# Performance work log

Hardware: AMD Instinct MI355X
Metric: run time of the kernel (lower is better)

## Reference

```python
import jax, jax.numpy as jnp
import numpy as np

E = 800_000
N = 50_000
NUM_RADIAL = 6
HIDDEN = 256
OUT_EMB = 192
OUT = 1
NUM_LAYERS = 3


def setup_inputs() -> dict:
    key = jax.random.key(0)
    ks = jax.random.split(key, 10)
    s = lambda fan_in: 1.0 / np.sqrt(fan_in)
    inp = {
        "x": jax.random.normal(ks[0], (E, HIDDEN), dtype=jnp.float32),
        "rbf": jax.random.normal(ks[1], (E, NUM_RADIAL), dtype=jnp.float32),
        "i": jax.random.randint(ks[2], (E,), 0, N, dtype=jnp.int64),
        "num_nodes": N,
        # params
        "W_rbf": jax.random.normal(ks[3], (NUM_RADIAL, HIDDEN), dtype=jnp.float32) * s(NUM_RADIAL),
        "W_up": jax.random.normal(ks[4], (HIDDEN, OUT_EMB), dtype=jnp.float32) * s(HIDDEN),
        "b_up": jnp.zeros((OUT_EMB,), dtype=jnp.float32),
        "W_lins": jax.random.normal(ks[5], (NUM_LAYERS, OUT_EMB, OUT_EMB), dtype=jnp.float32) * s(OUT_EMB),
        "b_lins": jnp.zeros((NUM_LAYERS, OUT_EMB), dtype=jnp.float32),
        "W_out": jax.random.normal(ks[6], (OUT_EMB, OUT), dtype=jnp.float32) * s(OUT_EMB),
    }
    return inp


def reference(x, rbf, i, num_nodes, W_rbf, W_up, b_up, W_lins, b_lins, W_out):
    # edge module: gate edge features by rbf projection
    g = jnp.matmul(rbf, W_rbf)          # [E, H]
    xe = g * x                          # [E, H]
    # scatter-add edges -> nodes
    xn = jax.ops.segment_sum(xe, i, num_segments=num_nodes)  # [N, H]
    # node MLP
    h = jnp.matmul(xn, W_up) + b_up     # [N, OUT_EMB]
    for l in range(W_lins.shape[0]):
        h = jax.nn.silu(jnp.matmul(h, W_lins[l]) + b_lins[l])
    return jnp.matmul(h, W_out)         # [N, OUT]
```

## Files before the change

### kernel.cpp

```cpp
#include <hip/hip_runtime.h>
#include <cmath>

#define HIDDEN 256
#define NUM_RADIAL 6
#define OUT_EMB 192
#define NUM_LAYERS 3
#define TN 32


__global__ __launch_bounds__(256) void hist_kernel(const int* __restrict__ idx,
                                                   int* __restrict__ counts, int E) {
    const int e = blockIdx.x * 256 + threadIdx.x;
    if (e < E) atomicAdd(&counts[idx[e]], 1);
}

__global__ __launch_bounds__(1024) void scan_kernel(const int* __restrict__ counts,
                                                    int* __restrict__ start,
                                                    int* __restrict__ cursor,
                                                    int N, int E) {
    __shared__ int pref[1024];
    const int t = threadIdx.x;
    const int chunk = (N + 1023) >> 10;
    const int lo = min(t * chunk, N), hi = min(lo + chunk, N);
    int s = 0;
    for (int i = lo; i < hi; i++) s += counts[i];
    pref[t] = s;
    __syncthreads();
    if (t == 0) {
        int run = 0;
        for (int i = 0; i < 1024; i++) { const int v = pref[i]; pref[i] = run; run += v; }
    }
    __syncthreads();
    int run = pref[t];
    for (int i = lo; i < hi; i++) {
        start[i] = run; cursor[i] = run; run += counts[i];
    }
    if (t == 0) start[N] = E;
}

__global__ __launch_bounds__(256) void perm_kernel(const int* __restrict__ idx,
                                                   int* __restrict__ cursor,
                                                   int* __restrict__ perm, int E) {
    const int e = blockIdx.x * 256 + threadIdx.x;
    if (e < E) {
        const int pos = atomicAdd(&cursor[idx[e]], 1);
        perm[pos] = e;
    }
}

__global__ __launch_bounds__(256) void gather_kernel(
    const float* __restrict__ x, const float* __restrict__ rbf,
    const int* __restrict__ perm, const int* __restrict__ start,
    const float* __restrict__ W_rbf, float* __restrict__ xn, int N)
{
    const int n = blockIdx.x;
    const int c = threadIdx.x;

    float wr[NUM_RADIAL];
    #pragma unroll
    for (int r = 0; r < NUM_RADIAL; r++) wr[r] = W_rbf[r * HIDDEN + c];

    const int p0 = start[n], p1 = start[n + 1];
    float acc = 0.f;
    for (int p = p0; p < p1; p++) {
        const int e = perm[p];
        float g = 0.f;
        #pragma unroll
        for (int r = 0; r < NUM_RADIAL; r++)
            g += wr[r] * rbf[(size_t)e * NUM_RADIAL + r];
        acc += g * x[(size_t)e * HIDDEN + c];
    }
    xn[(size_t)n * HIDDEN + c] = acc;
}


__global__ __launch_bounds__(192) void node_mlp(
    const float* __restrict__ xn,
    const float* __restrict__ W_up, const float* __restrict__ b_up,
    const float* __restrict__ W_lins, const float* __restrict__ b_lins,
    const float* __restrict__ W_out,
    float* __restrict__ out, int N)
{
    __shared__ float xl[TN * HIDDEN];
    __shared__ float hl[TN * OUT_EMB];
    const int j = threadIdx.x;
    const int nbase = blockIdx.x * TN;

    for (int t = j; t < TN * HIDDEN; t += 192) {
        const int n = t / HIDDEN;
        xl[t] = (nbase + n < N) ? xn[(size_t)(nbase + n) * HIDDEN + (t & (HIDDEN - 1))]
                                : 0.f;
    }
    __syncthreads();

    float acc[TN];

    {
        const float bj = b_up[j];
        #pragma unroll
        for (int n = 0; n < TN; n++) acc[n] = bj;
        for (int c0 = 0; c0 < HIDDEN; c0 += 32) {
            float w[32];
            #pragma unroll
            for (int k = 0; k < 32; k++) w[k] = W_up[(c0 + k) * OUT_EMB + j];
            #pragma unroll
            for (int k = 0; k < 32; k += 4) {
                #pragma unroll
                for (int n = 0; n < TN; n++) {
                    const float4 xv = *(const float4*)&xl[n * HIDDEN + c0 + k];
                    acc[n] += xv.x * w[k] + xv.y * w[k + 1] + xv.z * w[k + 2] + xv.w * w[k + 3];
                }
            }
        }
        __syncthreads();
        #pragma unroll
        for (int n = 0; n < TN; n++) hl[n * OUT_EMB + j] = acc[n];
        __syncthreads();
    }

    for (int l = 0; l < NUM_LAYERS; l++) {
        const float* __restrict__ W = W_lins + (size_t)l * OUT_EMB * OUT_EMB;
        const float bj = b_lins[l * OUT_EMB + j];
        #pragma unroll
        for (int n = 0; n < TN; n++) acc[n] = bj;
        for (int c0 = 0; c0 < OUT_EMB; c0 += 32) {
            float w[32];
            #pragma unroll
            for (int k = 0; k < 32; k++) w[k] = W[(c0 + k) * OUT_EMB + j];
            #pragma unroll
            for (int k = 0; k < 32; k += 4) {
                #pragma unroll
                for (int n = 0; n < TN; n++) {
                    const float4 hv = *(const float4*)&hl[n * OUT_EMB + c0 + k];
                    acc[n] += hv.x * w[k] + hv.y * w[k + 1] + hv.z * w[k + 2] + hv.w * w[k + 3];
                }
            }
        }
        __syncthreads();
        #pragma unroll
        for (int n = 0; n < TN; n++) {
            const float a = acc[n];
            hl[n * OUT_EMB + j] = a / (1.f + __expf(-a));
        }
        __syncthreads();
    }

    if (j < TN && nbase + j < N) {
        float s = 0.f;
        for (int c = 0; c < OUT_EMB; c++) s += hl[j * OUT_EMB + c] * W_out[c];
        out[nbase + j] = s;
    }
}

extern "C" void kernel_launch(void* const* d_in, const int* in_sizes, int n_in,
                              void* d_out, int out_size, void* d_ws, size_t ws_size,
                              hipStream_t stream) {
    const float* x      = (const float*)d_in[0];
    const float* rbf    = (const float*)d_in[1];
    const int*   idx    = (const int*)d_in[2];
    const float* W_rbf  = (const float*)d_in[4];
    const float* W_up   = (const float*)d_in[5];
    const float* b_up   = (const float*)d_in[6];
    const float* W_lins = (const float*)d_in[7];
    const float* b_lins = (const float*)d_in[8];
    const float* W_out  = (const float*)d_in[9];
    float* out = (float*)d_out;

    const int E = in_sizes[2];
    const int N = out_size;

    char* ws = (char*)d_ws;
    float* xn     = (float*)ws;                    ws += (size_t)N * HIDDEN * sizeof(float);
    int*   counts = (int*)ws;                      ws += (size_t)N * sizeof(int);
    int*   start  = (int*)ws;                      ws += (size_t)(N + 1) * sizeof(int);
    int*   cursor = (int*)ws;                      ws += (size_t)N * sizeof(int);
    int*   perm   = (int*)ws;

    hipMemsetAsync(counts, 0, (size_t)N * sizeof(int), stream);
    const int eblocks = (E + 255) / 256;
    hist_kernel<<<eblocks, 256, 0, stream>>>(idx, counts, E);
    scan_kernel<<<1, 1024, 0, stream>>>(counts, start, cursor, N, E);
    perm_kernel<<<eblocks, 256, 0, stream>>>(idx, cursor, perm, E);
    gather_kernel<<<N, 256, 0, stream>>>(x, rbf, perm, start, W_rbf, xn, N);

    node_mlp<<<(N + TN - 1) / TN, 192, 0, stream>>>(xn, W_up, b_up, W_lins, b_lins,
                                                    W_out, out, N);
}
```

Before: 2.155 ms.

## Vectorize gather per wavefront and retile node MLP with register blocking

The gather kernel now assigns one 64-lane wavefront per node, with each lane handling four channels through float4 loads, and processes two edges per iteration to expose more memory parallelism. The node MLP switches to 256 threads, where each thread computes an 8-node by 3-output register tile. The first layer reads xn directly from global memory instead of staging it in shared memory, which cuts the LDS footprint. The final output projection is split across 8 lanes per node and reduced with shuffles, replacing the mostly idle 32-thread serial loop. The trade-off is higher register pressure, and the up-projection now depends on global or cache reads of xn rather than LDS.

```diff
diff --git a/kernel.cpp b/kernel.cpp
--- a/kernel.cpp
+++ b/kernel.cpp
@@ -5,7 +5,10 @@
 #define NUM_RADIAL 6
 #define OUT_EMB 192
 #define NUM_LAYERS 3
-#define TN 32
+
+#define TM 32
+#define NPG 8
+#define JT 3
 
 
 __global__ __launch_bounds__(256) void hist_kernel(const int* __restrict__ idx,
@@ -48,107 +51,178 @@
     }
 }
 
+__device__ __forceinline__ float4 edge_term(const float rv0, const float rv1,
+                                            const float rv2, const float rv3,
+                                            const float rv4, const float rv5,
+                                            const float4* wr, const float4 xv) {
+    float4 g;
+    g.x = rv0*wr[0].x + rv1*wr[1].x + rv2*wr[2].x + rv3*wr[3].x + rv4*wr[4].x + rv5*wr[5].x;
+    g.y = rv0*wr[0].y + rv1*wr[1].y + rv2*wr[2].y + rv3*wr[3].y + rv4*wr[4].y + rv5*wr[5].y;
+    g.z = rv0*wr[0].z + rv1*wr[1].z + rv2*wr[2].z + rv3*wr[3].z + rv4*wr[4].z + rv5*wr[5].z;
+    g.w = rv0*wr[0].w + rv1*wr[1].w + rv2*wr[2].w + rv3*wr[3].w + rv4*wr[4].w + rv5*wr[5].w;
+    return make_float4(g.x*xv.x, g.y*xv.y, g.z*xv.z, g.w*xv.w);
+}
+
 __global__ __launch_bounds__(256) void gather_kernel(
     const float* __restrict__ x, const float* __restrict__ rbf,
     const int* __restrict__ perm, const int* __restrict__ start,
     const float* __restrict__ W_rbf, float* __restrict__ xn, int N)
 {
-    const int n = blockIdx.x;
-    const int c = threadIdx.x;
-
-    float wr[NUM_RADIAL];
+    const int lane = threadIdx.x & 63;
+    const int slot = threadIdx.x >> 6;
+    const int n = blockIdx.x * 4 + slot;
+    if (n >= N) return;
+    const int c0 = lane << 2;
+
+    float4 wr[NUM_RADIAL];
     #pragma unroll
-    for (int r = 0; r < NUM_RADIAL; r++) wr[r] = W_rbf[r * HIDDEN + c];
+    for (int r = 0; r < NUM_RADIAL; r++)
+        wr[r] = *(const float4*)&W_rbf[r * HIDDEN + c0];
 
     const int p0 = start[n], p1 = start[n + 1];
-    float acc = 0.f;
-    for (int p = p0; p < p1; p++) {
-        const int e = perm[p];
-        float g = 0.f;
-        #pragma unroll
-        for (int r = 0; r < NUM_RADIAL; r++)
-            g += wr[r] * rbf[(size_t)e * NUM_RADIAL + r];
-        acc += g * x[(size_t)e * HIDDEN + c];
-    }
-    xn[(size_t)n * HIDDEN + c] = acc;
-}
-
-
-__global__ __launch_bounds__(192) void node_mlp(
+    float4 acc = make_float4(0.f, 0.f, 0.f, 0.f);
+
+    int p = p0;
+    for (; p + 2 <= p1; p += 2) {
+        const int e0 = perm[p];
+        const int e1 = perm[p + 1];
+        const float2* rb0 = (const float2*)(rbf + (size_t)e0 * NUM_RADIAL);
+        const float2* rb1 = (const float2*)(rbf + (size_t)e1 * NUM_RADIAL);
+        const float2 a0 = rb0[0], a1 = rb0[1], a2 = rb0[2];
+        const float2 b0 = rb1[0], b1 = rb1[1], b2 = rb1[2];
+        const float4 xv0 = *(const float4*)&x[(size_t)e0 * HIDDEN + c0];
+        const float4 xv1 = *(const float4*)&x[(size_t)e1 * HIDDEN + c0];
+        const float4 t0 = edge_term(a0.x, a0.y, a1.x, a1.y, a2.x, a2.y, wr, xv0);
+        const float4 t1 = edge_term(b0.x, b0.y, b1.x, b1.y, b2.x, b2.y, wr, xv1);
+        acc.x += t0.x + t1.x; acc.y += t0.y + t1.y;
+        acc.z += t0.z + t1.z; acc.w += t0.w + t1.w;
+    }
+    if (p < p1) {
+        const int e0 = perm[p];
+        const float2* rb0 = (const float2*)(rbf + (size_t)e0 * NUM_RADIAL);
+        const float2 a0 = rb0[0], a1 = rb0[1], a2 = rb0[2];
+        const float4 xv0 = *(const float4*)&x[(size_t)e0 * HIDDEN + c0];
+        const float4 t0 = edge_term(a0.x, a0.y, a1.x, a1.y, a2.x, a2.y, wr, xv0);
+        acc.x += t0.x; acc.y += t0.y; acc.z += t0.z; acc.w += t0.w;
+    }
+    *(float4*)&xn[(size_t)n * HIDDEN + c0] = acc;
+}
+
+
+__global__ __launch_bounds__(256, 4) void node_mlp(
     const float* __restrict__ xn,
     const float* __restrict__ W_up, const float* __restrict__ b_up,
     const float* __restrict__ W_lins, const float* __restrict__ b_lins,
     const float* __restrict__ W_out,
     float* __restrict__ out, int N)
 {
-    __shared__ float xl[TN * HIDDEN];
-    __shared__ float hl[TN * OUT_EMB];
-    const int j = threadIdx.x;
-    const int nbase = blockIdx.x * TN;
-
-    for (int t = j; t < TN * HIDDEN; t += 192) {
-        const int n = t / HIDDEN;
-        xl[t] = (nbase + n < N) ? xn[(size_t)(nbase + n) * HIDDEN + (t & (HIDDEN - 1))]
-                                : 0.f;
-    }
-    __syncthreads();
-
-    float acc[TN];
+    __shared__ float hl[TM * OUT_EMB];
+    const int t = threadIdx.x;
+    const int j = t & 63;
+    const int g = t >> 6;
+    const int nbase = blockIdx.x * TM;
+    const int n0 = g * NPG;
+
+    float acc[NPG][JT];
+
+    const float* xrow[NPG];
+    #pragma unroll
+    for (int n = 0; n < NPG; n++) {
+        int nn = nbase + n0 + n;
+        if (nn > N - 1) nn = N - 1;
+        xrow[n] = xn + (size_t)nn * HIDDEN;
+    }
 
     {
-        const float bj = b_up[j];
-        #pragma unroll
-        for (int n = 0; n < TN; n++) acc[n] = bj;
-        for (int c0 = 0; c0 < HIDDEN; c0 += 32) {
-            float w[32];
-            #pragma unroll
-            for (int k = 0; k < 32; k++) w[k] = W_up[(c0 + k) * OUT_EMB + j];
-            #pragma unroll
-            for (int k = 0; k < 32; k += 4) {
-                #pragma unroll
-                for (int n = 0; n < TN; n++) {
-                    const float4 xv = *(const float4*)&xl[n * HIDDEN + c0 + k];
-                    acc[n] += xv.x * w[k] + xv.y * w[k + 1] + xv.z * w[k + 2] + xv.w * w[k + 3];
+        float bj[JT];
+        #pragma unroll
+        for (int m = 0; m < JT; m++) bj[m] = b_up[j + 64 * m];
+        #pragma unroll
+        for (int n = 0; n < NPG; n++)
+            #pragma unroll
+            for (int m = 0; m < JT; m++) acc[n][m] = bj[m];
+
+        for (int c0 = 0; c0 < HIDDEN; c0 += 8) {
+            float w[8][JT];
+            #pragma unroll
+            for (int k = 0; k < 8; k++)
+                #pragma unroll
+                for (int m = 0; m < JT; m++)
+                    w[k][m] = W_up[(c0 + k) * OUT_EMB + j + 64 * m];
+            #pragma unroll
+            for (int n = 0; n < NPG; n++) {
+                #pragma unroll
+                for (int k4 = 0; k4 < 8; k4 += 4) {
+                    const float4 xv = *(const float4*)(xrow[n] + c0 + k4);
+                    #pragma unroll
+                    for (int m = 0; m < JT; m++)
+                        acc[n][m] += xv.x * w[k4 + 0][m] + xv.y * w[k4 + 1][m]
+                                   + xv.z * w[k4 + 2][m] + xv.w * w[k4 + 3][m];
+                }
+            }
+        }
+        #pragma unroll
+        for (int n = 0; n < NPG; n++)
+            #pragma unroll
+            for (int m = 0; m < JT; m++)
+                hl[(n0 + n) * OUT_EMB + j + 64 * m] = acc[n][m];
+        __syncthreads();
+    }
+
+    for (int l = 0; l < NUM_LAYERS; l++) {
+        const float* __restrict__ W = W_lins + (size_t)l * OUT_EMB * OUT_EMB;
+        float bj[JT];
+        #pragma unroll
+        for (int m = 0; m < JT; m++) bj[m] = b_lins[l * OUT_EMB + j + 64 * m];
+        #pragma unroll
+        for (int n = 0; n < NPG; n++)
+            #pragma unroll
+            for (int m = 0; m < JT; m++) acc[n][m] = bj[m];
+
+        for (int c0 = 0; c0 < OUT_EMB; c0 += 8) {
+            float w[8][JT];
+            #pragma unroll
+            for (int k = 0; k < 8; k++)
+                #pragma unroll
+                for (int m = 0; m < JT; m++)
+                    w[k][m] = W[(c0 + k) * OUT_EMB + j + 64 * m];
+            #pragma unroll
+            for (int n = 0; n < NPG; n++) {
+                #pragma unroll
+                for (int k4 = 0; k4 < 8; k4 += 4) {
+                    const float4 hv = *(const float4*)&hl[(n0 + n) * OUT_EMB + c0 + k4];
+                    #pragma unroll
+                    for (int m = 0; m < JT; m++)
+                        acc[n][m] += hv.x * w[k4 + 0][m] + hv.y * w[k4 + 1][m]
+                                   + hv.z * w[k4 + 2][m] + hv.w * w[k4 + 3][m];
                 }
             }
         }
         __syncthreads();
         #pragma unroll
-        for (int n = 0; n < TN; n++) hl[n * OUT_EMB + j] = acc[n];
+        for (int n = 0; n < NPG; n++)
+            #pragma unroll
+            for (int m = 0; m < JT; m++) {
+                const float a = acc[n][m];
+                hl[(n0 + n) * OUT_EMB + j + 64 * m] = a / (1.f + __expf(-a));
+            }
         __syncthreads();
     }
 
-    for (int l = 0; l < NUM_LAYERS; l++) {
-        const float* __restrict__ W = W_lins + (size_t)l * OUT_EMB * OUT_EMB;
-        const float bj = b_lins[l * OUT_EMB + j];
-        #pragma unroll
-        for (int n = 0; n < TN; n++) acc[n] = bj;
-        for (int c0 = 0; c0 < OUT_EMB; c0 += 32) {
-            float w[32];
-            #pragma unroll
-            for (int k = 0; k < 32; k++) w[k] = W[(c0 + k) * OUT_EMB + j];
-            #pragma unroll
-            for (int k = 0; k < 32; k += 4) {
-                #pragma unroll
-                for (int n = 0; n < TN; n++) {
-                    const float4 hv = *(const float4*)&hl[n * OUT_EMB + c0 + k];
-                    acc[n] += hv.x * w[k] + hv.y * w[k + 1] + hv.z * w[k + 2] + hv.w * w[k + 3];
-                }
-            }
+    {
+        const int n = t >> 3;
+        const int sub = t & 7;
+        float s = 0.f;
+        #pragma unroll
+        for (int q = 0; q < 24; q += 4) {
+            const float4 hv = *(const float4*)&hl[n * OUT_EMB + sub * 24 + q];
+            const float4 wv = *(const float4*)&W_out[sub * 24 + q];
+            s += hv.x * wv.x + hv.y * wv.y + hv.z * wv.z + hv.w * wv.w;
         }
-        __syncthreads();
-        #pragma unroll
-        for (int n = 0; n < TN; n++) {
-            const float a = acc[n];
-            hl[n * OUT_EMB + j] = a / (1.f + __expf(-a));
-        }
-        __syncthreads();
-    }
-
-    if (j < TN && nbase + j < N) {
-        float s = 0.f;
-        for (int c = 0; c < OUT_EMB; c++) s += hl[j * OUT_EMB + c] * W_out[c];
-        out[nbase + j] = s;
+        s += __shfl_down(s, 4, 8);
+        s += __shfl_down(s, 2, 8);
+        s += __shfl_down(s, 1, 8);
+        if (sub == 0 && nbase + n < N) out[nbase + n] = s;
     }
 }
 
@@ -181,8 +255,8 @@
     hist_kernel<<<eblocks, 256, 0, stream>>>(idx, counts, E);
     scan_kernel<<<1, 1024, 0, stream>>>(counts, start, cursor, N, E);
     perm_kernel<<<eblocks, 256, 0, stream>>>(idx, cursor, perm, E);
-    gather_kernel<<<N, 256, 0, stream>>>(x, rbf, perm, start, W_rbf, xn, N);
-
-    node_mlp<<<(N + TN - 1) / TN, 192, 0, stream>>>(xn, W_up, b_up, W_lins, b_lins,
+    gather_kernel<<<(N + 3) / 4, 256, 0, stream>>>(x, rbf, perm, start, W_rbf, xn, N);
+
+    node_mlp<<<(N + TM - 1) / TM, 256, 0, stream>>>(xn, W_up, b_up, W_lins, b_lins,
                                                     W_out, out, N);
 }
```

Result: faster. 1.731 ms (-19.7%).
